# Performance work log

Hardware: AMD Instinct MI355X
Metric: run time of the kernel (lower is better)

Reference implementation:

```python
import jax, jax.numpy as jnp
import numpy as np

B, D, E, T = 262144, 128, 8, 3   # batch, input_dim, num_experts, num_tasks
H1, H2, G = 64, 32, 64           # expert hidden dims, gate hidden dim


def setup_inputs() -> dict:
    key = jax.random.key(0)
    ks = jax.random.split(key, 9)
    s = 0.05
    return {
        "x":   jax.random.normal(ks[0], (B, D), dtype=jnp.float32),
        # stacked expert MLP params: D -> H1 (relu) -> H2 (relu)
        "We1": jax.random.normal(ks[1], (E, D, H1), dtype=jnp.float32) * s,
        "be1": jax.random.normal(ks[2], (E, H1), dtype=jnp.float32) * s,
        "We2": jax.random.normal(ks[3], (E, H1, H2), dtype=jnp.float32) * s,
        "be2": jax.random.normal(ks[4], (E, H2), dtype=jnp.float32) * s,
        # stacked gate MLP params: D -> G (relu) -> E (linear, then softmax)
        "Wg1": jax.random.normal(ks[5], (T, D, G), dtype=jnp.float32) * s,
        "bg1": jax.random.normal(ks[6], (T, G), dtype=jnp.float32) * s,
        "Wg2": jax.random.normal(ks[7], (T, G, E), dtype=jnp.float32) * s,
        "bg2": jax.random.normal(ks[8], (T, E), dtype=jnp.float32) * s,
    }


def reference(x, We1, be1, We2, be2, Wg1, bg1, Wg2, bg2):
    # All experts as one batched GEMM chain: [B,E,H1] -> [B,E,H2]
    h1 = jax.nn.relu(jnp.einsum('bd,edh->beh', x, We1) + be1)
    experts_out = jax.nn.relu(jnp.einsum('beh,eho->beo', h1, We2) + be2)  # [B,E,H2]
    # All task gates as one batched GEMM chain: [B,T,E]
    g = jax.nn.relu(jnp.einsum('bd,tdh->bth', x, Wg1) + bg1)
    gate = jax.nn.softmax(jnp.einsum('bth,the->bte', g, Wg2) + bg2, axis=-1)
    # softmax-weighted sum over experts, per task
    out = jnp.einsum('bte,beo->bto', gate, experts_out)  # [B,T,H2]
    return tuple(out[:, t] for t in range(T))
```

## Files before the change

### kernel.cpp

```cpp
#include <hip/hip_runtime.h>

#define BROWS 262144
#define OUT_TASK_F32 8388608

#define WS_L1F 0
#define WS_L2F 196608
#define WS_B1  235520
#define WS_B2  238592

#define H1B 0
#define EOB 49152
#define SGB 81920
#define XSB 84992
#define LDS_TOTAL 93184

typedef __attribute__((ext_vector_type(8))) short bf16x8;
typedef __attribute__((ext_vector_type(4))) float f32x4;
typedef __attribute__((ext_vector_type(2))) unsigned int u32x2;

#define MFMA16(a, b, c) __builtin_amdgcn_mfma_f32_16x16x32_bf16((a), (b), (c), 0, 0, 0)

__device__ __forceinline__ unsigned short f2bf(float f) {
  unsigned int u = __float_as_uint(f);
  return (unsigned short)((u + 0x7FFFu + ((u >> 16) & 1u)) >> 16);
}
__device__ __forceinline__ unsigned int cvtpk(float lo, float hi) {
  unsigned int r;
  asm("v_cvt_pk_bf16_f32 %0, %1, %2" : "=v"(r) : "v"(lo), "v"(hi));
  return r;
}

__global__ void pack_kernel(const float* __restrict__ We1, const float* __restrict__ be1,
                            const float* __restrict__ We2, const float* __restrict__ be2,
                            const float* __restrict__ Wg1, const float* __restrict__ bg1,
                            const float* __restrict__ Wg2, const float* __restrict__ bg2,
                            unsigned char* __restrict__ ws) {
  int idx = blockIdx.x * blockDim.x + threadIdx.x;
  unsigned short* L1F = (unsigned short*)(ws + WS_L1F);
  unsigned short* L2F = (unsigned short*)(ws + WS_L2F);
  float* B1 = (float*)(ws + WS_B1);
  float* B2 = (float*)(ws + WS_B2);
  if (idx < 98304) {
    int j = idx & 7, lane = (idx >> 3) & 63, ks = (idx >> 9) & 3, nt = idx >> 11;
    int k = ks * 32 + ((lane >> 4) << 3) + j;
    int n = nt * 16 + (lane & 15);
    float v = 0.f;
    if (n < 512)      v = We1[((n >> 6) * 128 + k) * 64 + (n & 63)];
    else if (n < 704) v = Wg1[(((n - 512) >> 6) * 128 + k) * 64 + ((n - 512) & 63)];
    L1F[idx] = f2bf(v);
  } else if (idx < 98304 + 19456) {
    int i2 = idx - 98304;
    int j = i2 & 7, lane = (i2 >> 3) & 63, ks = (i2 >> 9) & 1, nt = i2 >> 10;
    int k = ks * 32 + ((lane >> 4) << 3) + j;
    int n = nt * 16 + (lane & 15);
    float v = 0.f;
    if (n < 256) v = We2[((n >> 5) * 64 + k) * 32 + (n & 31)];
    else { int g = n - 256, t = g >> 4, eo = g & 15; if (eo < 8) v = Wg2[(t * 64 + k) * 8 + eo]; }
    L2F[i2] = f2bf(v);
  } else if (idx < 98304 + 19456 + 768) {
    int n = idx - (98304 + 19456);
    float v = 0.f;
    if (n < 512)      v = be1[n];
    else if (n < 704) v = bg1[n - 512];
    B1[n] = v;
  } else if (idx < 98304 + 19456 + 768 + 304) {
    int n = idx - (98304 + 19456 + 768);
    float v = 0.f;
    if (n < 256) v = be2[n];
    else { int g = n - 256, t = g >> 4, eo = g & 15; if (eo < 8) v = bg2[t * 8 + eo]; }
    B2[n] = v;
  }
}

__global__ __launch_bounds__(512, 2) void mmoe_kernel(const float* __restrict__ x,
                                                      const unsigned char* __restrict__ ws,
                                                      float* __restrict__ out) {
  __shared__ unsigned char lds[LDS_TOTAL];

  const int tid = threadIdx.x;
  const int l   = tid & 63;
  const int wid = tid >> 6;
  const int l15 = l & 15;
  const int lhi = l >> 4;
  const int swz = (l15 & 7) << 4;

  const bf16x8* L1F = (const bf16x8*)(ws + WS_L1F);
  const bf16x8* L2F = (const bf16x8*)(ws + WS_L2F);
  const float*  B1  = (const float*)(ws + WS_B1);
  const float*  B2  = (const float*)(ws + WS_B2);

  int ntb[6];
#pragma unroll
  for (int i = 0; i < 6; ++i) ntb[i] = wid * 6 + i;
  if (wid >= 6) {
    int b = wid - 6;
#pragma unroll
    for (int i = 0; i < 4; ++i) ntb[i] = 36 + b * 4 + i;
    ntb[4] = 44 + b * 2; ntb[5] = 45 + b * 2;
  }

  bf16x8 w1f[6][4];
  f32x4 b1v[6];
#pragma unroll
  for (int i = 0; i < 6; ++i) {
#pragma unroll
    for (int ks = 0; ks < 4; ++ks) w1f[i][ks] = L1F[(ntb[i] * 4 + ks) * 64 + l];
    b1v[i] = *(const f32x4*)(B1 + ntb[i] * 16 + lhi * 4);
  }
  bf16x8 w2f[2][2];
  f32x4 b2v[2];
#pragma unroll
  for (int i = 0; i < 2; ++i) {
#pragma unroll
    for (int ks = 0; ks < 2; ++ks) w2f[i][ks] = L2F[((wid * 2 + i) * 2 + ks) * 64 + l];
    b2v[i] = *(const f32x4*)(B2 + wid * 32 + i * 16 + lhi * 4);
  }
  bf16x8 wgf[2];
  f32x4 bgv = (f32x4){0.f, 0.f, 0.f, 0.f};
  if (wid >= 5) {
    int t = wid - 5;
#pragma unroll
    for (int ks = 0; ks < 2; ++ks) wgf[ks] = L2F[((16 + t) * 2 + ks) * 64 + l];
    bgv = *(const f32x4*)(B2 + 256 + t * 16 + lhi * 4);
  }

  const int srow = tid >> 5, sk4 = tid & 31;
  const int rowbase = blockIdx.x * 1024;
  const int sswz = (srow & 7) << 4;

  {
    float4 sv = *(const float4*)(x + (size_t)(rowbase + srow) * 128 + sk4 * 4);
    u32x2 p; p[0] = cvtpk(sv.x, sv.y); p[1] = cvtpk(sv.z, sv.w);
    *(u32x2*)(lds + XSB + ((srow * 256 + sk4 * 8) ^ sswz)) = p;
  }
  __syncthreads();

#pragma unroll 1
  for (int s = 0; s < 66; ++s) {
    const int pL1 = s & 1;
    const int pL2 = (s - 1) & 1;

    float4 sv;
    const bool stage = (s + 1 < 64);
    if (stage)
      sv = *(const float4*)(x + (size_t)(rowbase + (s + 1) * 16 + srow) * 128 + sk4 * 4);

    if (s >= 2 && wid < 6) {
      int t = wid >> 1, hf = wid & 1;
      f32x4 pA = *(const f32x4*)(lds + SGB + pL1 * 1536 + l15 * 96 + t * 32);
      f32x4 pB = *(const f32x4*)(lds + SGB + pL1 * 1536 + l15 * 96 + t * 32 + 16);
      f32x4 vac = (f32x4){0.f, 0.f, 0.f, 0.f};
#pragma unroll
      for (int e = 0; e < 4; ++e)
        vac += pA[e] * (*(const f32x4*)(lds + EOB + pL1 * 16384 + l15 * 1024 +
                                        ((e * 128 + hf * 64 + lhi * 16) ^ swz)));
#pragma unroll
      for (int e = 0; e < 4; ++e)
        vac += pB[e] * (*(const f32x4*)(lds + EOB + pL1 * 16384 + l15 * 1024 +
                                        (((e + 4) * 128 + hf * 64 + lhi * 16) ^ swz)));
      float* op = out + (size_t)t * OUT_TASK_F32 +
                  (size_t)(rowbase + (s - 2) * 16 + l15) * 32 + hf * 16 + lhi * 4;
      *(float4*)op = (float4){vac[0], vac[1], vac[2], vac[3]};
    }

    if (s < 64) {
      bf16x8 xa[4];
#pragma unroll
      for (int ks = 0; ks < 4; ++ks)
        xa[ks] = *(const bf16x8*)(lds + XSB + pL1 * 4096 + l15 * 256 +
                                  ((ks * 64 + lhi * 16) ^ swz));
      f32x4 acc[6];
#pragma unroll
      for (int i = 0; i < 6; ++i) acc[i] = b1v[i];
#pragma unroll
      for (int ks = 0; ks < 4; ++ks)
#pragma unroll
        for (int i = 0; i < 6; ++i)
          acc[i] = MFMA16(w1f[i][ks], xa[ks], acc[i]);
#pragma unroll
      for (int i = 0; i < 6; ++i) {
        u32x2 p;
        p[0] = cvtpk(fmaxf(acc[i][0], 0.f), fmaxf(acc[i][1], 0.f));
        p[1] = cvtpk(fmaxf(acc[i][2], 0.f), fmaxf(acc[i][3], 0.f));
        *(u32x2*)(lds + H1B + pL1 * 24576 + l15 * 1536 + ((ntb[i] * 32 + lhi * 8) ^ swz)) = p;
      }
    }

    if (s >= 1 && s < 65) {
      bf16x8 hb0 = *(const bf16x8*)(lds + H1B + pL2 * 24576 + l15 * 1536 + ((wid * 128 + lhi * 16) ^ swz));
      bf16x8 hb1 = *(const bf16x8*)(lds + H1B + pL2 * 24576 + l15 * 1536 + ((wid * 128 + 64 + lhi * 16) ^ swz));
      f32x4 a2[2] = {b2v[0], b2v[1]};
#pragma unroll
      for (int i = 0; i < 2; ++i) {
        a2[i] = MFMA16(w2f[i][0], hb0, a2[i]);
        a2[i] = MFMA16(w2f[i][1], hb1, a2[i]);
        f32x4 r;
        r[0] = fmaxf(a2[i][0], 0.f); r[1] = fmaxf(a2[i][1], 0.f);
        r[2] = fmaxf(a2[i][2], 0.f); r[3] = fmaxf(a2[i][3], 0.f);
        *(f32x4*)(lds + EOB + pL2 * 16384 + l15 * 1024 + ((wid * 128 + i * 64 + lhi * 16) ^ swz)) = r;
      }
      if (wid >= 5) {
        int t = wid - 5;
        bf16x8 gb0 = *(const bf16x8*)(lds + H1B + pL2 * 24576 + l15 * 1536 + ((1024 + t * 128 + lhi * 16) ^ swz));
        bf16x8 gb1 = *(const bf16x8*)(lds + H1B + pL2 * 24576 + l15 * 1536 + ((1024 + t * 128 + 64 + lhi * 16) ^ swz));
        f32x4 ag = bgv;
        ag = MFMA16(wgf[0], gb0, ag);
        ag = MFMA16(wgf[1], gb1, ag);
        float s0 = ag[0], s1 = ag[1], s2 = ag[2], s3 = ag[3];
        float o0 = __shfl_xor(s0, 16), o1 = __shfl_xor(s1, 16);
        float o2 = __shfl_xor(s2, 16), o3 = __shfl_xor(s3, 16);
        float mx = fmaxf(fmaxf(fmaxf(s0, s1), fmaxf(s2, s3)),
                         fmaxf(fmaxf(o0, o1), fmaxf(o2, o3)));
        float q0 = __expf(s0 - mx), q1 = __expf(s1 - mx), q2 = __expf(s2 - mx), q3 = __expf(s3 - mx);
        float ps = q0 + q1 + q2 + q3;
        float inv = 1.f / (ps + __shfl_xor(ps, 16));
        if (lhi < 2)
          *(f32x4*)(lds + SGB + pL2 * 1536 + l15 * 96 + t * 32 + lhi * 16) =
              (f32x4){q0 * inv, q1 * inv, q2 * inv, q3 * inv};
      }
    }

    if (stage) {
      u32x2 p; p[0] = cvtpk(sv.x, sv.y); p[1] = cvtpk(sv.z, sv.w);
      *(u32x2*)(lds + XSB + pL2 * 4096 + ((srow * 256 + sk4 * 8) ^ sswz)) = p;
    }

    __syncthreads();
  }
}

extern "C" void kernel_launch(void* const* d_in, const int* in_sizes, int n_in,
                              void* d_out, int out_size, void* d_ws, size_t ws_size,
                              hipStream_t stream) {
  const float* x   = (const float*)d_in[0];
  const float* We1 = (const float*)d_in[1];
  const float* be1 = (const float*)d_in[2];
  const float* We2 = (const float*)d_in[3];
  const float* be2 = (const float*)d_in[4];
  const float* Wg1 = (const float*)d_in[5];
  const float* bg1 = (const float*)d_in[6];
  const float* Wg2 = (const float*)d_in[7];
  const float* bg2 = (const float*)d_in[8];
  unsigned char* ws = (unsigned char*)d_ws;
  float* out = (float*)d_out;

  pack_kernel<<<465, 256, 0, stream>>>(We1, be1, We2, be2, Wg1, bg1, Wg2, bg2, ws);
  mmoe_kernel<<<256, 512, 0, stream>>>(x, ws, out);
}
```

Before: 103.2 us.

## Load x directly into MFMA fragments and store expert outputs as bf16

Drops the LDS staging buffer for x. Each wave now loads its x rows from global memory straight into registers in the MFMA operand layout and converts them to bf16 there, instead of cooperatively staging the next tile through LDS. Expert outputs are also stored in LDS as bf16 rather than fp32, halving that buffer, and are unpacked to fp32 in the gated sum. Together these cut total LDS use, which may allow more blocks per CU. The cost is losing the one-step prefetch of x, so global load latency is now exposed within the same iteration, and expert outputs take an extra rounding to bf16 before the weighted sum.

```diff
diff --git a/kernel.cpp b/kernel.cpp
--- a/kernel.cpp
+++ b/kernel.cpp
@@ -10,13 +10,13 @@
 
 #define H1B 0
 #define EOB 49152
-#define SGB 81920
-#define XSB 84992
-#define LDS_TOTAL 93184
+#define SGB 65536
+#define LDS_TOTAL 68608
 
 typedef __attribute__((ext_vector_type(8))) short bf16x8;
 typedef __attribute__((ext_vector_type(4))) float f32x4;
 typedef __attribute__((ext_vector_type(2))) unsigned int u32x2;
+typedef __attribute__((ext_vector_type(4))) unsigned int u32x4;
 
 #define MFMA16(a, b, c) __builtin_amdgcn_mfma_f32_16x16x32_bf16((a), (b), (c), 0, 0, 0)
 
@@ -124,26 +124,22 @@
     bgv = *(const f32x4*)(B2 + 256 + t * 16 + lhi * 4);
   }
 
-  const int srow = tid >> 5, sk4 = tid & 31;
   const int rowbase = blockIdx.x * 1024;
-  const int sswz = (srow & 7) << 4;
-
-  {
-    float4 sv = *(const float4*)(x + (size_t)(rowbase + srow) * 128 + sk4 * 4);
-    u32x2 p; p[0] = cvtpk(sv.x, sv.y); p[1] = cvtpk(sv.z, sv.w);
-    *(u32x2*)(lds + XSB + ((srow * 256 + sk4 * 8) ^ sswz)) = p;
-  }
-  __syncthreads();
 
 #pragma unroll 1
   for (int s = 0; s < 66; ++s) {
     const int pL1 = s & 1;
     const int pL2 = (s - 1) & 1;
 
-    float4 sv;
-    const bool stage = (s + 1 < 64);
-    if (stage)
-      sv = *(const float4*)(x + (size_t)(rowbase + (s + 1) * 16 + srow) * 128 + sk4 * 4);
+    float4 xf[8];
+    if (s < 64) {
+      const float* xp = x + (size_t)(rowbase + s * 16 + l15) * 128 + lhi * 8;
+#pragma unroll
+      for (int ks = 0; ks < 4; ++ks) {
+        xf[2 * ks]     = *(const float4*)(xp + ks * 32);
+        xf[2 * ks + 1] = *(const float4*)(xp + ks * 32 + 4);
+      }
+    }
 
     if (s >= 2 && wid < 6) {
       int t = wid >> 1, hf = wid & 1;
@@ -151,13 +147,15 @@
       f32x4 pB = *(const f32x4*)(lds + SGB + pL1 * 1536 + l15 * 96 + t * 32 + 16);
       f32x4 vac = (f32x4){0.f, 0.f, 0.f, 0.f};
 #pragma unroll
-      for (int e = 0; e < 4; ++e)
-        vac += pA[e] * (*(const f32x4*)(lds + EOB + pL1 * 16384 + l15 * 1024 +
-                                        ((e * 128 + hf * 64 + lhi * 16) ^ swz)));
-#pragma unroll
-      for (int e = 0; e < 4; ++e)
-        vac += pB[e] * (*(const f32x4*)(lds + EOB + pL1 * 16384 + l15 * 1024 +
-                                        (((e + 4) * 128 + hf * 64 + lhi * 16) ^ swz)));
+      for (int e = 0; e < 8; ++e) {
+        float g = (e < 4) ? pA[e & 3] : pB[e & 3];
+        u32x2 q = *(const u32x2*)(lds + EOB + pL1 * 8192 + l15 * 512 +
+                                  ((e * 64 + hf * 32 + lhi * 8) ^ swz));
+        vac[0] += g * __uint_as_float(q[0] << 16);
+        vac[1] += g * __uint_as_float(q[0] & 0xffff0000u);
+        vac[2] += g * __uint_as_float(q[1] << 16);
+        vac[3] += g * __uint_as_float(q[1] & 0xffff0000u);
+      }
       float* op = out + (size_t)t * OUT_TASK_F32 +
                   (size_t)(rowbase + (s - 2) * 16 + l15) * 32 + hf * 16 + lhi * 4;
       *(float4*)op = (float4){vac[0], vac[1], vac[2], vac[3]};
@@ -166,9 +164,13 @@
     if (s < 64) {
       bf16x8 xa[4];
 #pragma unroll
-      for (int ks = 0; ks < 4; ++ks)
-        xa[ks] = *(const bf16x8*)(lds + XSB + pL1 * 4096 + l15 * 256 +
-                                  ((ks * 64 + lhi * 16) ^ swz));
+      for (int ks = 0; ks < 4; ++ks) {
+        float4 a = xf[2 * ks], b = xf[2 * ks + 1];
+        u32x4 u;
+        u[0] = cvtpk(a.x, a.y); u[1] = cvtpk(a.z, a.w);
+        u[2] = cvtpk(b.x, b.y); u[3] = cvtpk(b.z, b.w);
+        xa[ks] = *(bf16x8*)&u;
+      }
       f32x4 acc[6];
 #pragma unroll
       for (int i = 0; i < 6; ++i) acc[i] = b1v[i];
@@ -194,10 +196,10 @@
       for (int i = 0; i < 2; ++i) {
         a2[i] = MFMA16(w2f[i][0], hb0, a2[i]);
         a2[i] = MFMA16(w2f[i][1], hb1, a2[i]);
-        f32x4 r;
-        r[0] = fmaxf(a2[i][0], 0.f); r[1] = fmaxf(a2[i][1], 0.f);
-        r[2] = fmaxf(a2[i][2], 0.f); r[3] = fmaxf(a2[i][3], 0.f);
-        *(f32x4*)(lds + EOB + pL2 * 16384 + l15 * 1024 + ((wid * 128 + i * 64 + lhi * 16) ^ swz)) = r;
+        u32x2 p;
+        p[0] = cvtpk(fmaxf(a2[i][0], 0.f), fmaxf(a2[i][1], 0.f));
+        p[1] = cvtpk(fmaxf(a2[i][2], 0.f), fmaxf(a2[i][3], 0.f));
+        *(u32x2*)(lds + EOB + pL2 * 8192 + l15 * 512 + ((wid * 64 + i * 32 + lhi * 8) ^ swz)) = p;
       }
       if (wid >= 5) {
         int t = wid - 5;
@@ -220,11 +222,6 @@
       }
     }
 
-    if (stage) {
-      u32x2 p; p[0] = cvtpk(sv.x, sv.y); p[1] = cvtpk(sv.z, sv.w);
-      *(u32x2*)(lds + XSB + pL2 * 4096 + ((srow * 256 + sk4 * 8) ^ sswz)) = p;
-    }
-
     __syncthreads();
   }
 }
```

After: 193.3 us. +87.3%, slower.

## Double block to 1024 threads and split per-wave MFMA work in half

Applied to the files above, without the earlier changes.

Doubles the workgroup from 8 to 16 waves and redistributes the work: each wave now computes 3 layer-1 N-tiles instead of 6, one layer-2 tile instead of two, and half as many combine outputs, with x staging done as float2 per lane. Fewer weight fragments are held per wave, which cuts register pressure and raises the number of waves per CU available to hide LDS and global latency. In exchange, the block-wide barrier now has to synchronise twice as many waves every step, and stores become narrower (float2 instead of float4).

```diff
diff --git a/kernel.cpp b/kernel.cpp
--- a/kernel.cpp
+++ b/kernel.cpp
@@ -16,6 +16,7 @@
 
 typedef __attribute__((ext_vector_type(8))) short bf16x8;
 typedef __attribute__((ext_vector_type(4))) float f32x4;
+typedef __attribute__((ext_vector_type(2))) float f32x2;
 typedef __attribute__((ext_vector_type(2))) unsigned int u32x2;
 
 #define MFMA16(a, b, c) __builtin_amdgcn_mfma_f32_16x16x32_bf16((a), (b), (c), 0, 0, 0)
@@ -72,9 +73,9 @@
   }
 }
 
-__global__ __launch_bounds__(512, 2) void mmoe_kernel(const float* __restrict__ x,
-                                                      const unsigned char* __restrict__ ws,
-                                                      float* __restrict__ out) {
+__global__ __launch_bounds__(1024) void mmoe_kernel(const float* __restrict__ x,
+                                                    const unsigned char* __restrict__ ws,
+                                                    float* __restrict__ out) {
   __shared__ unsigned char lds[LDS_TOTAL];
 
   const int tid = threadIdx.x;
@@ -89,49 +90,34 @@
   const float*  B1  = (const float*)(ws + WS_B1);
   const float*  B2  = (const float*)(ws + WS_B2);
 
-  int ntb[6];
-#pragma unroll
-  for (int i = 0; i < 6; ++i) ntb[i] = wid * 6 + i;
-  if (wid >= 6) {
-    int b = wid - 6;
-#pragma unroll
-    for (int i = 0; i < 4; ++i) ntb[i] = 36 + b * 4 + i;
-    ntb[4] = 44 + b * 2; ntb[5] = 45 + b * 2;
-  }
-
-  bf16x8 w1f[6][4];
-  f32x4 b1v[6];
-#pragma unroll
-  for (int i = 0; i < 6; ++i) {
-#pragma unroll
-    for (int ks = 0; ks < 4; ++ks) w1f[i][ks] = L1F[(ntb[i] * 4 + ks) * 64 + l];
-    b1v[i] = *(const f32x4*)(B1 + ntb[i] * 16 + lhi * 4);
-  }
-  bf16x8 w2f[2][2];
-  f32x4 b2v[2];
-#pragma unroll
-  for (int i = 0; i < 2; ++i) {
-#pragma unroll
-    for (int ks = 0; ks < 2; ++ks) w2f[i][ks] = L2F[((wid * 2 + i) * 2 + ks) * 64 + l];
-    b2v[i] = *(const f32x4*)(B2 + wid * 32 + i * 16 + lhi * 4);
-  }
+  bf16x8 w1f[3][4];
+  f32x4 b1v[3];
+#pragma unroll
+  for (int i = 0; i < 3; ++i) {
+#pragma unroll
+    for (int ks = 0; ks < 4; ++ks) w1f[i][ks] = L1F[((wid * 3 + i) * 4 + ks) * 64 + l];
+    b1v[i] = *(const f32x4*)(B1 + (wid * 3 + i) * 16 + lhi * 4);
+  }
+  bf16x8 w2f[2];
+#pragma unroll
+  for (int ks = 0; ks < 2; ++ks) w2f[ks] = L2F[(wid * 2 + ks) * 64 + l];
+  f32x4 b2v = *(const f32x4*)(B2 + wid * 16 + lhi * 4);
+
   bf16x8 wgf[2];
   f32x4 bgv = (f32x4){0.f, 0.f, 0.f, 0.f};
-  if (wid >= 5) {
-    int t = wid - 5;
+  if (wid >= 13) {
+    int t = wid - 13;
 #pragma unroll
     for (int ks = 0; ks < 2; ++ks) wgf[ks] = L2F[((16 + t) * 2 + ks) * 64 + l];
     bgv = *(const f32x4*)(B2 + 256 + t * 16 + lhi * 4);
   }
 
-  const int srow = tid >> 5, sk4 = tid & 31;
+  const int sboff = wid * 256 + ((l * 4) ^ ((wid & 7) << 4));
   const int rowbase = blockIdx.x * 1024;
-  const int sswz = (srow & 7) << 4;
 
   {
-    float4 sv = *(const float4*)(x + (size_t)(rowbase + srow) * 128 + sk4 * 4);
-    u32x2 p; p[0] = cvtpk(sv.x, sv.y); p[1] = cvtpk(sv.z, sv.w);
-    *(u32x2*)(lds + XSB + ((srow * 256 + sk4 * 8) ^ sswz)) = p;
+    float2 v = *(const float2*)(x + (size_t)(rowbase + wid) * 128 + l * 2);
+    *(unsigned int*)(lds + XSB + sboff) = cvtpk(v.x, v.y);
   }
   __syncthreads();
 
@@ -140,69 +126,68 @@
     const int pL1 = s & 1;
     const int pL2 = (s - 1) & 1;
 
-    float4 sv;
+    float2 sv;
     const bool stage = (s + 1 < 64);
     if (stage)
-      sv = *(const float4*)(x + (size_t)(rowbase + (s + 1) * 16 + srow) * 128 + sk4 * 4);
-
-    if (s >= 2 && wid < 6) {
-      int t = wid >> 1, hf = wid & 1;
+      sv = *(const float2*)(x + (size_t)(rowbase + (s + 1) * 16 + wid) * 128 + l * 2);
+
+    if (s >= 2 && wid < 12) {
+      int t = wid >> 2, q = wid & 3;
       f32x4 pA = *(const f32x4*)(lds + SGB + pL1 * 1536 + l15 * 96 + t * 32);
       f32x4 pB = *(const f32x4*)(lds + SGB + pL1 * 1536 + l15 * 96 + t * 32 + 16);
-      f32x4 vac = (f32x4){0.f, 0.f, 0.f, 0.f};
-#pragma unroll
-      for (int e = 0; e < 4; ++e)
-        vac += pA[e] * (*(const f32x4*)(lds + EOB + pL1 * 16384 + l15 * 1024 +
-                                        ((e * 128 + hf * 64 + lhi * 16) ^ swz)));
-#pragma unroll
-      for (int e = 0; e < 4; ++e)
-        vac += pB[e] * (*(const f32x4*)(lds + EOB + pL1 * 16384 + l15 * 1024 +
-                                        (((e + 4) * 128 + hf * 64 + lhi * 16) ^ swz)));
+      f32x2 vac = (f32x2){0.f, 0.f};
+#pragma unroll
+      for (int e = 0; e < 8; ++e) {
+        float g = (e < 4) ? pA[e & 3] : pB[e & 3];
+        f32x2 eo = *(const f32x2*)(lds + EOB + pL1 * 16384 + l15 * 1024 +
+                                   ((e * 128 + q * 32 + lhi * 8) ^ swz));
+        vac += g * eo;
+      }
       float* op = out + (size_t)t * OUT_TASK_F32 +
-                  (size_t)(rowbase + (s - 2) * 16 + l15) * 32 + hf * 16 + lhi * 4;
-      *(float4*)op = (float4){vac[0], vac[1], vac[2], vac[3]};
+                  (size_t)(rowbase + (s - 2) * 16 + l15) * 32 + q * 8 + lhi * 2;
+      *(float2*)op = (float2){vac[0], vac[1]};
     }
 
     if (s < 64) {
-      bf16x8 xa[4];
-#pragma unroll
-      for (int ks = 0; ks < 4; ++ks)
-        xa[ks] = *(const bf16x8*)(lds + XSB + pL1 * 4096 + l15 * 256 +
-                                  ((ks * 64 + lhi * 16) ^ swz));
-      f32x4 acc[6];
-#pragma unroll
-      for (int i = 0; i < 6; ++i) acc[i] = b1v[i];
-#pragma unroll
-      for (int ks = 0; ks < 4; ++ks)
-#pragma unroll
-        for (int i = 0; i < 6; ++i)
-          acc[i] = MFMA16(w1f[i][ks], xa[ks], acc[i]);
-#pragma unroll
-      for (int i = 0; i < 6; ++i) {
+      f32x4 acc[3] = {b1v[0], b1v[1], b1v[2]};
+#pragma unroll
+      for (int ks = 0; ks < 4; ++ks) {
+        bf16x8 xa = *(const bf16x8*)(lds + XSB + pL1 * 4096 + l15 * 256 +
+                                     ((ks * 64 + lhi * 16) ^ swz));
+#pragma unroll
+        for (int i = 0; i < 3; ++i) acc[i] = MFMA16(w1f[i][ks], xa, acc[i]);
+      }
+#pragma unroll
+      for (int i = 0; i < 3; ++i) {
         u32x2 p;
         p[0] = cvtpk(fmaxf(acc[i][0], 0.f), fmaxf(acc[i][1], 0.f));
         p[1] = cvtpk(fmaxf(acc[i][2], 0.f), fmaxf(acc[i][3], 0.f));
-        *(u32x2*)(lds + H1B + pL1 * 24576 + l15 * 1536 + ((ntb[i] * 32 + lhi * 8) ^ swz)) = p;
+        *(u32x2*)(lds + H1B + pL1 * 24576 + l15 * 1536 +
+                  (((wid * 3 + i) * 32 + lhi * 8) ^ swz)) = p;
       }
     }
 
     if (s >= 1 && s < 65) {
-      bf16x8 hb0 = *(const bf16x8*)(lds + H1B + pL2 * 24576 + l15 * 1536 + ((wid * 128 + lhi * 16) ^ swz));
-      bf16x8 hb1 = *(const bf16x8*)(lds + H1B + pL2 * 24576 + l15 * 1536 + ((wid * 128 + 64 + lhi * 16) ^ swz));
-      f32x4 a2[2] = {b2v[0], b2v[1]};
-#pragma unroll
-      for (int i = 0; i < 2; ++i) {
-        a2[i] = MFMA16(w2f[i][0], hb0, a2[i]);
-        a2[i] = MFMA16(w2f[i][1], hb1, a2[i]);
-        f32x4 r;
-        r[0] = fmaxf(a2[i][0], 0.f); r[1] = fmaxf(a2[i][1], 0.f);
-        r[2] = fmaxf(a2[i][2], 0.f); r[3] = fmaxf(a2[i][3], 0.f);
-        *(f32x4*)(lds + EOB + pL2 * 16384 + l15 * 1024 + ((wid * 128 + i * 64 + lhi * 16) ^ swz)) = r;
-      }
-      if (wid >= 5) {
-        int t = wid - 5;
-        bf16x8 gb0 = *(const bf16x8*)(lds + H1B + pL2 * 24576 + l15 * 1536 + ((1024 + t * 128 + lhi * 16) ^ swz));
-        bf16x8 gb1 = *(const bf16x8*)(lds + H1B + pL2 * 24576 + l15 * 1536 + ((1024 + t * 128 + 64 + lhi * 16) ^ swz));
+      const int e = wid >> 1;
+      bf16x8 hb0 = *(const bf16x8*)(lds + H1B + pL2 * 24576 + l15 * 1536 +
+                                    ((e * 128 + lhi * 16) ^ swz));
+      bf16x8 hb1 = *(const bf16x8*)(lds + H1B + pL2 * 24576 + l15 * 1536 +
+                                    ((e * 128 + 64 + lhi * 16) ^ swz));
+      f32x4 a2 = b2v;
+      a2 = MFMA16(w2f[0], hb0, a2);
+      a2 = MFMA16(w2f[1], hb1, a2);
+      f32x4 r;
+      r[0] = fmaxf(a2[0], 0.f); r[1] = fmaxf(a2[1], 0.f);
+      r[2] = fmaxf(a2[2], 0.f); r[3] = fmaxf(a2[3], 0.f);
+      *(f32x4*)(lds + EOB + pL2 * 16384 + l15 * 1024 +
+                ((e * 128 + (wid & 1) * 64 + lhi * 16) ^ swz)) = r;
+
+      if (wid >= 13) {
+        int t = wid - 13;
+        bf16x8 gb0 = *(const bf16x8*)(lds + H1B + pL2 * 24576 + l15 * 1536 +
+                                      ((1024 + t * 128 + lhi * 16) ^ swz));
+        bf16x8 gb1 = *(const bf16x8*)(lds + H1B + pL2 * 24576 + l15 * 1536 +
+                                      ((1024 + t * 128 + 64 + lhi * 16) ^ swz));
         f32x4 ag = bgv;
         ag = MFMA16(wgf[0], gb0, ag);
         ag = MFMA16(wgf[1], gb1, ag);
@@ -211,7 +196,8 @@
         float o2 = __shfl_xor(s2, 16), o3 = __shfl_xor(s3, 16);
         float mx = fmaxf(fmaxf(fmaxf(s0, s1), fmaxf(s2, s3)),
                          fmaxf(fmaxf(o0, o1), fmaxf(o2, o3)));
-        float q0 = __expf(s0 - mx), q1 = __expf(s1 - mx), q2 = __expf(s2 - mx), q3 = __expf(s3 - mx);
+        float q0 = __expf(s0 - mx), q1 = __expf(s1 - mx);
+        float q2 = __expf(s2 - mx), q3 = __expf(s3 - mx);
         float ps = q0 + q1 + q2 + q3;
         float inv = 1.f / (ps + __shfl_xor(ps, 16));
         if (lhi < 2)
@@ -220,10 +206,8 @@
       }
     }
 
-    if (stage) {
-      u32x2 p; p[0] = cvtpk(sv.x, sv.y); p[1] = cvtpk(sv.z, sv.w);
-      *(u32x2*)(lds + XSB + pL2 * 4096 + ((srow * 256 + sk4 * 8) ^ sswz)) = p;
-    }
+    if (stage)
+      *(unsigned int*)(lds + XSB + pL2 * 4096 + sboff) = cvtpk(sv.x, sv.y);
 
     __syncthreads();
   }
@@ -245,5 +229,5 @@
   float* out = (float*)d_out;
 
   pack_kernel<<<465, 256, 0, stream>>>(We1, be1, We2, be2, Wg1, bg1, Wg2, bg2, ws);
-  mmoe_kernel<<<256, 512, 0, stream>>>(x, ws, out);
-}
+  mmoe_kernel<<<256, 1024, 0, stream>>>(x, ws, out);
+}
```

After: 124.4 us. 1.2x slower.
